# Optimization experiments

Hardware: AMD Instinct MI355X
Metric: run time of the kernel (lower is better)

## Reference

```python
import jax, jax.numpy as jnp
import numpy as np

B, S, H, D, DM = 2, 512, 8, 32, 256  # batch, seq_len, n_head, d_k, d_model


def setup_inputs() -> dict:
    key = jax.random.key(0)
    ks = jax.random.split(key, 8)
    scale = 0.02
    return {
        "hidden_states": jax.random.normal(ks[0], (B, S, DM), dtype=jnp.float32),
        "rpe": jax.random.normal(ks[1], (B, S, S, D), dtype=jnp.float32),
        "w_q": jax.random.normal(ks[2], (DM, H * D), dtype=jnp.float32) * scale,
        "w_k": jax.random.normal(ks[3], (DM, H * D), dtype=jnp.float32) * scale,
        "w_v": jax.random.normal(ks[4], (DM, H * D), dtype=jnp.float32) * scale,
        "fc_w": jax.random.normal(ks[5], (H * D, DM), dtype=jnp.float32) * scale,
        "fc_b": jnp.zeros((DM,), dtype=jnp.float32),
        "ln_w": jnp.ones((DM,), dtype=jnp.float32),
        "ln_b": jnp.zeros((DM,), dtype=jnp.float32),
        "station_num": 256,
    }


def reference(hidden_states, rpe, w_q, w_k, w_v, fc_w, fc_b, ln_w, ln_b, station_num):
    b, s, dm = hidden_states.shape
    d = rpe.shape[-1]
    h = w_q.shape[1] // d

    def heads(x, w):
        # (b, s, dm) @ (dm, h*d) -> (b, h, s, d)
        return (x @ w).reshape(b, s, h, d).transpose(0, 2, 1, 3)

    q = heads(hidden_states, w_q)
    k = heads(hidden_states, w_k)
    v = heads(hidden_states, w_v)

    # torch: (q.unsqueeze(2) * k.unsqueeze(3) * rpe.unsqueeze(1)).sum(-1)
    # scores[b,h,i,j] = sum_d q[b,h,j,d] * k[b,h,i,d] * rpe[b,i,j,d]
    scores = jnp.einsum('bhjd,bhid,bijd->bhij', q, k, rpe) / jnp.sqrt(jnp.float32(d))

    # shielded mask: column j visible if j < station_num, plus the diagonal
    col = jnp.arange(s) < station_num                  # (s,)
    mask = col[None, :] | jnp.eye(s, dtype=bool)        # (s, s)
    scores = jnp.where(mask[None, None], scores, jnp.float32(-1e10))

    attn = jax.nn.softmax(scores, axis=-1)              # (b, h, s, s)
    out = jnp.einsum('bhij,bhjd->bhid', attn, v)        # (b, h, s, d)
    out = out.transpose(0, 2, 1, 3).reshape(b, s, h * d)

    ctx = out @ fc_w + fc_b + hidden_states             # residual
    mu = jnp.mean(ctx, axis=-1, keepdims=True)
    var = jnp.mean(jnp.square(ctx - mu), axis=-1, keepdims=True)
    ctx = (ctx - mu) / jnp.sqrt(var + 1e-6) * ln_w + ln_b
    return ctx
```

## Files before the change

kernel.cpp:

```cpp
#include <hip/hip_runtime.h>
#include <hip/hip_bf16.h>

#define B_  2
#define S_  512
#define H_  8
#define D_  32
#define DM_ 256
#define HD_ 256
#define NROW 4
#define TI  8
#define PSTR 520

__global__ __launch_bounds__(256) void qkv_kernel(
    const float* __restrict__ hid, const float* __restrict__ wq,
    const float* __restrict__ wk, const float* __restrict__ wv,
    float* __restrict__ qo, float* __restrict__ ko, float* __restrict__ vo)
{
  __shared__ float hs[NROW][DM_];
  const int r0 = blockIdx.x * NROW;
  const float* w   = (blockIdx.y == 0) ? wq : (blockIdx.y == 1) ? wk : wv;
  float*       out = (blockIdx.y == 0) ? qo : (blockIdx.y == 1) ? ko : vo;
  const int tid = threadIdx.x;

  for (int idx = tid; idx < NROW * DM_; idx += 256)
    hs[idx >> 8][idx & 255] = hid[r0 * DM_ + idx];
  __syncthreads();

  float acc[NROW] = {0.f, 0.f, 0.f, 0.f};
  const float* wp = w + tid;
  #pragma unroll 8
  for (int c4 = 0; c4 < DM_ / 4; ++c4) {
    const float w0 = wp[(4 * c4 + 0) * HD_];
    const float w1 = wp[(4 * c4 + 1) * HD_];
    const float w2 = wp[(4 * c4 + 2) * HD_];
    const float w3 = wp[(4 * c4 + 3) * HD_];
    #pragma unroll
    for (int r = 0; r < NROW; ++r) {
      const float4 hv = reinterpret_cast<const float4*>(&hs[r][0])[c4];
      acc[r] = fmaf(hv.x, w0, acc[r]);
      acc[r] = fmaf(hv.y, w1, acc[r]);
      acc[r] = fmaf(hv.z, w2, acc[r]);
      acc[r] = fmaf(hv.w, w3, acc[r]);
    }
  }
  const int h = tid >> 5, d = tid & 31;
  #pragma unroll
  for (int r = 0; r < NROW; ++r) {
    const int g = r0 + r;
    const int b = g >> 9, s = g & (S_ - 1);
    out[((b * H_ + h) * S_ + s) * D_ + d] = acc[r];
  }
}

__global__ __launch_bounds__(512) void attn_kernel(
    const float* __restrict__ rpe, const float* __restrict__ q_ws,
    const float* __restrict__ k_ws, const float* __restrict__ v_ws,
    const int* __restrict__ station_p, float* __restrict__ o_ws)
{
  __shared__ float k_lds[TI * D_];
  __shared__ float p_lds[TI][PSTR];
  __shared__ float sums[TI];
  __shared__ float4 red[8][64];

  const int tid = threadIdx.x;
  const int b  = blockIdx.x;
  const int i0 = blockIdx.y * TI;
  const int h  = blockIdx.z;
  int station = station_p[0];
  if (station > S_) station = S_;
  if (station < 0)  station = 0;

  if (tid < TI * D_)
    k_lds[tid] = k_ws[((b * H_ + h) * S_ + i0 + (tid >> 5)) * D_ + (tid & 31)];
  __syncthreads();

  const int j = tid;
  const bool jlt = (j < station);
  const bool intile = (j >= i0) && (j < i0 + TI);

  float4 qv[8];
  if (jlt || intile) {
    const float4* qp = reinterpret_cast<const float4*>(
        q_ws + ((b * H_ + h) * S_ + j) * D_);
    #pragma unroll
    for (int t = 0; t < 8; ++t) qv[t] = qp[t];
  }

  const float4* rbase = reinterpret_cast<const float4*>(
      rpe + (((size_t)b * S_ + i0) * S_ + j) * D_);
  const int rstride = S_ * D_ / 4;

  float4 rcur[8];
  if (jlt || (j == i0)) {
    #pragma unroll
    for (int t = 0; t < 8; ++t) rcur[t] = rbase[t];
  }
  #pragma unroll
  for (int ii = 0; ii < TI; ++ii) {
    const int i = i0 + ii;
    const bool ok = jlt || (j == i);
    float4 rnext[8];
    if (ii < TI - 1 && (jlt || (j == i + 1))) {
      const float4* rp = rbase + (ii + 1) * rstride;
      #pragma unroll
      for (int t = 0; t < 8; ++t) rnext[t] = rp[t];
    }
    float s = -1e30f;
    if (ok) {
      const float4* kp = reinterpret_cast<const float4*>(&k_lds[ii * D_]);
      float acc = 0.f;
      #pragma unroll
      for (int t = 0; t < 8; ++t) {
        const float4 kv = kp[t];
        acc = fmaf(qv[t].x * kv.x, rcur[t].x, acc);
        acc = fmaf(qv[t].y * kv.y, rcur[t].y, acc);
        acc = fmaf(qv[t].z * kv.z, rcur[t].z, acc);
        acc = fmaf(qv[t].w * kv.w, rcur[t].w, acc);
      }
      s = acc * 0.17677669529663687f;
    }
    p_lds[ii][j] = s;
    #pragma unroll
    for (int t = 0; t < 8; ++t) rcur[t] = rnext[t];
  }
  __syncthreads();

  {
    const int w = tid >> 6, lane = tid & 63;
    float m = -1e30f;
    #pragma unroll
    for (int jj = lane; jj < S_; jj += 64) m = fmaxf(m, p_lds[w][jj]);
    #pragma unroll
    for (int o = 32; o; o >>= 1) m = fmaxf(m, __shfl_xor(m, o, 64));
    float sum = 0.f;
    #pragma unroll
    for (int jj = lane; jj < S_; jj += 64) {
      const float p = __expf(p_lds[w][jj] - m);
      p_lds[w][jj] = p;
      sum += p;
    }
    #pragma unroll
    for (int o = 32; o; o >>= 1) sum += __shfl_xor(sum, o, 64);
    if (lane == 0) sums[w] = sum;
  }
  __syncthreads();

  {
    const int part = tid >> 6;
    const int t    = tid & 63;
    const int ii = t >> 3, d4 = t & 7;
    const float4* vp = reinterpret_cast<const float4*>(
        v_ws + ((size_t)(b * H_ + h) * S_) * D_) + d4;
    float4 acc = {0.f, 0.f, 0.f, 0.f};
    #pragma unroll 4
    for (int jj = part; jj < station; jj += 8) {
      const float p = p_lds[ii][jj];
      const float4 v = vp[jj * (D_ / 4)];
      acc.x = fmaf(p, v.x, acc.x);
      acc.y = fmaf(p, v.y, acc.y);
      acc.z = fmaf(p, v.z, acc.z);
      acc.w = fmaf(p, v.w, acc.w);
    }
    const int ig = i0 + ii;
    if (ig >= station && part == (ig & 7)) {
      const float p = p_lds[ii][ig];
      const float4 v = vp[ig * (D_ / 4)];
      acc.x = fmaf(p, v.x, acc.x);
      acc.y = fmaf(p, v.y, acc.y);
      acc.z = fmaf(p, v.z, acc.z);
      acc.w = fmaf(p, v.w, acc.w);
    }
    red[part][t] = acc;
  }
  __syncthreads();
  if (tid < 64) {
    const int ii = tid >> 3, d4 = tid & 7;
    float4 a = red[0][tid];
    #pragma unroll
    for (int p = 1; p < 8; ++p) {
      const float4 r = red[p][tid];
      a.x += r.x; a.y += r.y; a.z += r.z; a.w += r.w;
    }
    const float inv = 1.f / sums[ii];
    a.x *= inv; a.y *= inv; a.z *= inv; a.w *= inv;
    reinterpret_cast<float4*>(
        o_ws + ((b * H_ + h) * S_ + i0 + ii) * D_)[d4] = a;
  }
}

__global__ __launch_bounds__(256) void fc_ln_kernel(
    const float* __restrict__ o_ws, const float* __restrict__ fc_w,
    const float* __restrict__ fc_b, const float* __restrict__ hid,
    const float* __restrict__ ln_w, const float* __restrict__ ln_b,
    float* __restrict__ out)
{
  __shared__ float orow[NROW][HD_];
  __shared__ float red[NROW][4];
  const int tid = threadIdx.x;
  const int r0 = blockIdx.x * NROW;

  for (int idx = tid; idx < NROW * HD_; idx += 256) {
    const int r = idx >> 8, m = idx & 255;
    const int g = r0 + r;
    const int b = g >> 9, i = g & (S_ - 1);
    orow[r][m] = o_ws[((b * H_ + (m >> 5)) * S_ + i) * D_ + (m & 31)];
  }
  __syncthreads();

  float acc[NROW] = {0.f, 0.f, 0.f, 0.f};
  const float* wp = fc_w + tid;
  #pragma unroll 8
  for (int n4 = 0; n4 < HD_ / 4; ++n4) {
    const float w0 = wp[(4 * n4 + 0) * DM_];
    const float w1 = wp[(4 * n4 + 1) * DM_];
    const float w2 = wp[(4 * n4 + 2) * DM_];
    const float w3 = wp[(4 * n4 + 3) * DM_];
    #pragma unroll
    for (int r = 0; r < NROW; ++r) {
      const float4 ov = reinterpret_cast<const float4*>(&orow[r][0])[n4];
      acc[r] = fmaf(ov.x, w0, acc[r]);
      acc[r] = fmaf(ov.y, w1, acc[r]);
      acc[r] = fmaf(ov.z, w2, acc[r]);
      acc[r] = fmaf(ov.w, w3, acc[r]);
    }
  }
  const float bias = fc_b[tid];
  #pragma unroll
  for (int r = 0; r < NROW; ++r) acc[r] += bias + hid[(r0 + r) * DM_ + tid];

  const int w = tid >> 6, lane = tid & 63;
  float mu[NROW];
  #pragma unroll
  for (int r = 0; r < NROW; ++r) {
    float s = acc[r];
    #pragma unroll
    for (int o = 32; o; o >>= 1) s += __shfl_xor(s, o, 64);
    if (lane == 0) red[r][w] = s;
  }
  __syncthreads();
  #pragma unroll
  for (int r = 0; r < NROW; ++r)
    mu[r] = (red[r][0] + red[r][1] + red[r][2] + red[r][3]) * (1.f / DM_);
  __syncthreads();
  #pragma unroll
  for (int r = 0; r < NROW; ++r) {
    const float dd = acc[r] - mu[r];
    float s = dd * dd;
    #pragma unroll
    for (int o = 32; o; o >>= 1) s += __shfl_xor(s, o, 64);
    if (lane == 0) red[r][w] = s;
  }
  __syncthreads();
  const float lw = ln_w[tid], lb = ln_b[tid];
  #pragma unroll
  for (int r = 0; r < NROW; ++r) {
    const float var = (red[r][0] + red[r][1] + red[r][2] + red[r][3]) * (1.f / DM_);
    out[(r0 + r) * DM_ + tid] =
        (acc[r] - mu[r]) * rsqrtf(var + 1e-6f) * lw + lb;
  }
}

extern "C" void kernel_launch(void* const* d_in, const int* in_sizes, int n_in,
                              void* d_out, int out_size, void* d_ws, size_t ws_size,
                              hipStream_t stream) {
  const float* hid = (const float*)d_in[0];
  const float* rpe = (const float*)d_in[1];
  const float* wq  = (const float*)d_in[2];
  const float* wk  = (const float*)d_in[3];
  const float* wv  = (const float*)d_in[4];
  const float* fcw = (const float*)d_in[5];
  const float* fcb = (const float*)d_in[6];
  const float* lnw = (const float*)d_in[7];
  const float* lnb = (const float*)d_in[8];
  const int* station = (const int*)d_in[9];
  float* out = (float*)d_out;

  const size_t per = (size_t)B_ * H_ * S_ * D_;
  float* q_ws = (float*)d_ws;
  float* k_ws = q_ws + per;
  float* v_ws = k_ws + per;
  float* o_ws = v_ws + per;

  dim3 gA(B_ * S_ / NROW, 3);
  qkv_kernel<<<gA, 256, 0, stream>>>(hid, wq, wk, wv, q_ws, k_ws, v_ws);
  dim3 gB(B_, S_ / TI, H_);
  attn_kernel<<<gB, 512, 0, stream>>>(rpe, q_ws, k_ws, v_ws, station, o_ws);
  fc_ln_kernel<<<B_ * S_ / NROW, 256, 0, stream>>>(o_ws, fcw, fcb, hid, lnw, lnb, out);
}
```

Baseline: 181.1 us.

## Process two heads per attention block to reuse each rpe load

```diff
diff --git a/kernel.cpp b/kernel.cpp
--- a/kernel.cpp
+++ b/kernel.cpp
@@ -9,6 +9,8 @@
 #define HD_ 256
 #define NROW 4
 #define TI  8
+#define HC  2
+#define NR  (TI * HC)
 #define PSTR 520
 
 __global__ __launch_bounds__(256) void qkv_kernel(
@@ -52,139 +54,156 @@
   }
 }
 
-__global__ __launch_bounds__(512) void attn_kernel(
+__global__ __launch_bounds__(512, 2) void attn_kernel(
     const float* __restrict__ rpe, const float* __restrict__ q_ws,
     const float* __restrict__ k_ws, const float* __restrict__ v_ws,
     const int* __restrict__ station_p, float* __restrict__ o_ws)
 {
-  __shared__ float k_lds[TI * D_];
-  __shared__ float p_lds[TI][PSTR];
-  __shared__ float sums[TI];
-  __shared__ float4 red[8][64];
+  __shared__ float k_lds[NR * D_];
+  __shared__ float p_lds[NR][PSTR];
+  __shared__ float sums[NR];
+  __shared__ float4 redv[8][NR][8];
 
   const int tid = threadIdx.x;
-  const int b  = blockIdx.x;
-  const int i0 = blockIdx.y * TI;
-  const int h  = blockIdx.z;
+  const int n   = blockIdx.x;
+  const int hg  = (n >> 3) & 3;
+  const int t   = (n & 7) | ((n >> 5) << 3);
+  const int b   = t >> 6;
+  const int i0  = (t & 63) * TI;
+  const int h0  = hg * HC;
+
   int station = station_p[0];
   if (station > S_) station = S_;
   if (station < 0)  station = 0;
 
-  if (tid < TI * D_)
-    k_lds[tid] = k_ws[((b * H_ + h) * S_ + i0 + (tid >> 5)) * D_ + (tid & 31)];
+  {
+    const int r = tid >> 5, d = tid & 31;
+    const int hh = r >> 3, ii = r & 7;
+    k_lds[tid] = k_ws[((b * H_ + h0 + hh) * S_ + i0 + ii) * D_ + d];
+  }
   __syncthreads();
 
   const int j = tid;
   const bool jlt = (j < station);
   const bool intile = (j >= i0) && (j < i0 + TI);
 
-  float4 qv[8];
+  float4 q0[8], q1[8];
   if (jlt || intile) {
-    const float4* qp = reinterpret_cast<const float4*>(
-        q_ws + ((b * H_ + h) * S_ + j) * D_);
-    #pragma unroll
-    for (int t = 0; t < 8; ++t) qv[t] = qp[t];
+    const float4* qp0 = reinterpret_cast<const float4*>(
+        q_ws + ((b * H_ + h0 + 0) * S_ + j) * D_);
+    const float4* qp1 = reinterpret_cast<const float4*>(
+        q_ws + ((b * H_ + h0 + 1) * S_ + j) * D_);
+    #pragma unroll
+    for (int tt = 0; tt < 8; ++tt) { q0[tt] = qp0[tt]; q1[tt] = qp1[tt]; }
   }
 
   const float4* rbase = reinterpret_cast<const float4*>(
       rpe + (((size_t)b * S_ + i0) * S_ + j) * D_);
   const int rstride = S_ * D_ / 4;
 
-  float4 rcur[8];
-  if (jlt || (j == i0)) {
-    #pragma unroll
-    for (int t = 0; t < 8; ++t) rcur[t] = rbase[t];
-  }
   #pragma unroll
   for (int ii = 0; ii < TI; ++ii) {
     const int i = i0 + ii;
     const bool ok = jlt || (j == i);
-    float4 rnext[8];
-    if (ii < TI - 1 && (jlt || (j == i + 1))) {
-      const float4* rp = rbase + (ii + 1) * rstride;
-      #pragma unroll
-      for (int t = 0; t < 8; ++t) rnext[t] = rp[t];
-    }
-    float s = -1e30f;
+    float s0 = -1e30f, s1 = -1e30f;
     if (ok) {
-      const float4* kp = reinterpret_cast<const float4*>(&k_lds[ii * D_]);
-      float acc = 0.f;
-      #pragma unroll
-      for (int t = 0; t < 8; ++t) {
-        const float4 kv = kp[t];
-        acc = fmaf(qv[t].x * kv.x, rcur[t].x, acc);
-        acc = fmaf(qv[t].y * kv.y, rcur[t].y, acc);
-        acc = fmaf(qv[t].z * kv.z, rcur[t].z, acc);
-        acc = fmaf(qv[t].w * kv.w, rcur[t].w, acc);
+      const float4* rp  = rbase + ii * rstride;
+      const float4* kp0 = reinterpret_cast<const float4*>(&k_lds[(0 * TI + ii) * D_]);
+      const float4* kp1 = reinterpret_cast<const float4*>(&k_lds[(1 * TI + ii) * D_]);
+      float a0 = 0.f, a1 = 0.f;
+      #pragma unroll
+      for (int tt = 0; tt < 8; ++tt) {
+        const float4 rv = rp[tt];
+        const float4 k0 = kp0[tt];
+        const float4 k1 = kp1[tt];
+        a0 = fmaf(q0[tt].x * k0.x, rv.x, a0);
+        a0 = fmaf(q0[tt].y * k0.y, rv.y, a0);
+        a0 = fmaf(q0[tt].z * k0.z, rv.z, a0);
+        a0 = fmaf(q0[tt].w * k0.w, rv.w, a0);
+        a1 = fmaf(q1[tt].x * k1.x, rv.x, a1);
+        a1 = fmaf(q1[tt].y * k1.y, rv.y, a1);
+        a1 = fmaf(q1[tt].z * k1.z, rv.z, a1);
+        a1 = fmaf(q1[tt].w * k1.w, rv.w, a1);
       }
-      s = acc * 0.17677669529663687f;
-    }
-    p_lds[ii][j] = s;
-    #pragma unroll
-    for (int t = 0; t < 8; ++t) rcur[t] = rnext[t];
+      s0 = a0 * 0.17677669529663687f;
+      s1 = a1 * 0.17677669529663687f;
+    }
+    p_lds[0 * TI + ii][j] = s0;
+    p_lds[1 * TI + ii][j] = s1;
   }
   __syncthreads();
 
   {
     const int w = tid >> 6, lane = tid & 63;
-    float m = -1e30f;
-    #pragma unroll
-    for (int jj = lane; jj < S_; jj += 64) m = fmaxf(m, p_lds[w][jj]);
-    #pragma unroll
-    for (int o = 32; o; o >>= 1) m = fmaxf(m, __shfl_xor(m, o, 64));
-    float sum = 0.f;
-    #pragma unroll
-    for (int jj = lane; jj < S_; jj += 64) {
-      const float p = __expf(p_lds[w][jj] - m);
-      p_lds[w][jj] = p;
-      sum += p;
-    }
-    #pragma unroll
-    for (int o = 32; o; o >>= 1) sum += __shfl_xor(sum, o, 64);
-    if (lane == 0) sums[w] = sum;
+    for (int rr = w; rr < NR; rr += 8) {
+      float m = -1e30f;
+      #pragma unroll
+      for (int jj = lane; jj < S_; jj += 64) m = fmaxf(m, p_lds[rr][jj]);
+      #pragma unroll
+      for (int o = 32; o; o >>= 1) m = fmaxf(m, __shfl_xor(m, o, 64));
+      float sum = 0.f;
+      #pragma unroll
+      for (int jj = lane; jj < S_; jj += 64) {
+        const float p = __expf(p_lds[rr][jj] - m);
+        p_lds[rr][jj] = p;
+        sum += p;
+      }
+      #pragma unroll
+      for (int o = 32; o; o >>= 1) sum += __shfl_xor(sum, o, 64);
+      if (lane == 0) sums[rr] = sum;
+    }
   }
   __syncthreads();
 
   {
     const int part = tid >> 6;
-    const int t    = tid & 63;
-    const int ii = t >> 3, d4 = t & 7;
-    const float4* vp = reinterpret_cast<const float4*>(
-        v_ws + ((size_t)(b * H_ + h) * S_) * D_) + d4;
-    float4 acc = {0.f, 0.f, 0.f, 0.f};
+    const int lane = tid & 63;
+    const int ii = lane >> 3, d4 = lane & 7;
+    const float4* vp0 = reinterpret_cast<const float4*>(
+        v_ws + ((size_t)(b * H_ + h0 + 0) * S_) * D_) + d4;
+    const float4* vp1 = reinterpret_cast<const float4*>(
+        v_ws + ((size_t)(b * H_ + h0 + 1) * S_) * D_) + d4;
+    float4 a0 = {0.f, 0.f, 0.f, 0.f};
+    float4 a1 = {0.f, 0.f, 0.f, 0.f};
     #pragma unroll 4
     for (int jj = part; jj < station; jj += 8) {
-      const float p = p_lds[ii][jj];
-      const float4 v = vp[jj * (D_ / 4)];
-      acc.x = fmaf(p, v.x, acc.x);
-      acc.y = fmaf(p, v.y, acc.y);
-      acc.z = fmaf(p, v.z, acc.z);
-      acc.w = fmaf(p, v.w, acc.w);
+      const float p0 = p_lds[0 * TI + ii][jj];
+      const float p1 = p_lds[1 * TI + ii][jj];
+      const float4 v0 = vp0[jj * (D_ / 4)];
+      const float4 v1 = vp1[jj * (D_ / 4)];
+      a0.x = fmaf(p0, v0.x, a0.x); a0.y = fmaf(p0, v0.y, a0.y);
+      a0.z = fmaf(p0, v0.z, a0.z); a0.w = fmaf(p0, v0.w, a0.w);
+      a1.x = fmaf(p1, v1.x, a1.x); a1.y = fmaf(p1, v1.y, a1.y);
+      a1.z = fmaf(p1, v1.z, a1.z); a1.w = fmaf(p1, v1.w, a1.w);
     }
     const int ig = i0 + ii;
     if (ig >= station && part == (ig & 7)) {
-      const float p = p_lds[ii][ig];
-      const float4 v = vp[ig * (D_ / 4)];
-      acc.x = fmaf(p, v.x, acc.x);
-      acc.y = fmaf(p, v.y, acc.y);
-      acc.z = fmaf(p, v.z, acc.z);
-      acc.w = fmaf(p, v.w, acc.w);
-    }
-    red[part][t] = acc;
-  }
-  __syncthreads();
-  if (tid < 64) {
-    const int ii = tid >> 3, d4 = tid & 7;
-    float4 a = red[0][tid];
+      const float p0 = p_lds[0 * TI + ii][ig];
+      const float p1 = p_lds[1 * TI + ii][ig];
+      const float4 v0 = vp0[ig * (D_ / 4)];
+      const float4 v1 = vp1[ig * (D_ / 4)];
+      a0.x = fmaf(p0, v0.x, a0.x); a0.y = fmaf(p0, v0.y, a0.y);
+      a0.z = fmaf(p0, v0.z, a0.z); a0.w = fmaf(p0, v0.w, a0.w);
+      a1.x = fmaf(p1, v1.x, a1.x); a1.y = fmaf(p1, v1.y, a1.y);
+      a1.z = fmaf(p1, v1.z, a1.z); a1.w = fmaf(p1, v1.w, a1.w);
+    }
+    redv[part][0 * TI + ii][d4] = a0;
+    redv[part][1 * TI + ii][d4] = a1;
+  }
+  __syncthreads();
+  if (tid < NR * 8) {
+    const int r = tid >> 3, d4 = tid & 7;
+    float4 a = redv[0][r][d4];
     #pragma unroll
     for (int p = 1; p < 8; ++p) {
-      const float4 r = red[p][tid];
-      a.x += r.x; a.y += r.y; a.z += r.z; a.w += r.w;
-    }
-    const float inv = 1.f / sums[ii];
+      const float4 x = redv[p][r][d4];
+      a.x += x.x; a.y += x.y; a.z += x.z; a.w += x.w;
+    }
+    const float inv = 1.f / sums[r];
     a.x *= inv; a.y *= inv; a.z *= inv; a.w *= inv;
+    const int hh = r >> 3, ii = r & 7;
     reinterpret_cast<float4*>(
-        o_ws + ((b * H_ + h) * S_ + i0 + ii) * D_)[d4] = a;
+        o_ws + ((b * H_ + h0 + hh) * S_ + i0 + ii) * D_)[d4] = a;
   }
 }
 
@@ -283,7 +302,7 @@
 
   dim3 gA(B_ * S_ / NROW, 3);
   qkv_kernel<<<gA, 256, 0, stream>>>(hid, wq, wk, wv, q_ws, k_ws, v_ws);
-  dim3 gB(B_, S_ / TI, H_);
-  attn_kernel<<<gB, 512, 0, stream>>>(rpe, q_ws, k_ws, v_ws, station, o_ws);
+  attn_kernel<<<B_ * (S_ / TI) * (H_ / HC), 512, 0, stream>>>(
+      rpe, q_ws, k_ws, v_ws, station, o_ws);
   fc_ln_kernel<<<B_ * S_ / NROW, 256, 0, stream>>>(o_ws, fcw, fcb, hid, lnw, lnb, out);
 }
```

Result: faster. 168.4 us (-7.0%).
